# Performance work log

Hardware: AMD Instinct MI355X
Metric: run time of the kernel (lower is better)

## Reference

```python
import jax, jax.numpy as jnp
import numpy as np

B, CIN, COUT, HID, H, W, K, PAD = 16, 64, 64, 32, 32, 32, 5, 2


def self_attention(x, Wq, Wk, Wv):
    # x: [B,C,H,W]; Wq,Wk: [HID,C]; Wv: [C,C]  (1x1 convs as channel matmuls)
    b, c, h, w = x.shape
    n = h * w
    xf = x.reshape(b, c, n)                      # [B,C,N]
    q = jnp.einsum('dc,bcn->bdn', Wq, xf)        # [B,HID,N]
    k = jnp.einsum('dc,bcn->bdn', Wk, xf)        # [B,HID,N]
    v = jnp.einsum('ec,bcn->ben', Wv, xf)        # [B,C,N]
    scores = jnp.einsum('bdn,bdm->bnm', q, k)    # [B,N,N]
    attn = jax.nn.softmax(scores, axis=-1)
    out = jnp.einsum('bcm,bnm->bcn', v, attn)    # aggregate values
    out = out.reshape(b, c, h, w)
    return x + out, attn                          # residual


def conv_lstm_cell(x, h, c, W_lstm, b_lstm):
    combined = jnp.concatenate([x, h], axis=1)   # [B,CIN+COUT,H,W]
    gates = jax.lax.conv_general_dilated(
        combined, W_lstm, window_strides=(1, 1),
        padding=[(PAD, PAD), (PAD, PAD)],
        dimension_numbers=('NCHW', 'OIHW', 'NCHW'))
    gates = gates + b_lstm[None, :, None, None]
    i, f, o, g = jnp.split(gates, 4, axis=1)
    i, f, o = jax.nn.sigmoid(i), jax.nn.sigmoid(f), jax.nn.sigmoid(o)
    g = jnp.tanh(g)
    c_new = f * c + i * g
    h_new = o * jnp.tanh(c_new)
    return h_new, c_new


def setup_inputs() -> dict:
    key = jax.random.key(0)
    ks = jax.random.split(key, 12)
    s = 0.05
    return {
        'x': jax.random.normal(ks[0], (B, CIN, H, W), jnp.float32),
        'h': jax.random.normal(ks[1], (B, COUT, H, W), jnp.float32),
        'c': jax.random.normal(ks[2], (B, COUT, H, W), jnp.float32),
        'Wq_x': jax.random.normal(ks[3], (HID, CIN), jnp.float32) * s,
        'Wk_x': jax.random.normal(ks[4], (HID, CIN), jnp.float32) * s,
        'Wv_x': jax.random.normal(ks[5], (CIN, CIN), jnp.float32) * s,
        'Wq_h': jax.random.normal(ks[6], (HID, COUT), jnp.float32) * s,
        'Wk_h': jax.random.normal(ks[7], (HID, COUT), jnp.float32) * s,
        'Wv_h': jax.random.normal(ks[8], (COUT, COUT), jnp.float32) * s,
        'W_lstm': jax.random.normal(ks[9], (4 * COUT, CIN + COUT, K, K), jnp.float32) * s,
        'b_lstm': jnp.zeros((4 * COUT,), jnp.float32),
    }


def reference(x, h, c, Wq_x, Wk_x, Wv_x, Wq_h, Wk_h, Wv_h, W_lstm, b_lstm):
    X, _ = self_attention(x, Wq_x, Wk_x, Wv_x)
    new_h, new_c = conv_lstm_cell(X, h, c, W_lstm, b_lstm)
    new_h, atten = self_attention(new_h, Wq_h, Wk_h, Wv_h)
    new_h = new_h + new_h  # faithful to `new_h += new_h`
    return new_h, new_c, atten
```

## Files before the change

kernel.cpp:

```cpp
#include <hip/hip_runtime.h>
#include <hip/hip_bf16.h>
#include <cstddef>
#include <cstdint>

#define NTOK 1024
#define NB   16
#define NC   64
#define NHID 32

#define PAD_BSTRIDE 165888
#define PAD_KSTRIDE 82944
#define PAD_BYTES   5308416

typedef __attribute__((ext_vector_type(8))) short short8;
typedef __attribute__((ext_vector_type(4))) float f32x4;

__device__ __forceinline__ ushort f2b(float f) {
  uint32_t u = __builtin_bit_cast(uint32_t, f);
  return (ushort)((u + 0x7FFFu + ((u >> 16) & 1u)) >> 16);
}
__device__ __forceinline__ float b2f(ushort u) {
  return __builtin_bit_cast(float, (uint32_t)u << 16);
}
__device__ __forceinline__ short8 ldw8(const float* __restrict__ p) {
  float4 f0 = *(const float4*)p, f1 = *(const float4*)(p + 4);
  short8 r;
  r[0] = (short)f2b(f0.x); r[1] = (short)f2b(f0.y);
  r[2] = (short)f2b(f0.z); r[3] = (short)f2b(f0.w);
  r[4] = (short)f2b(f1.x); r[5] = (short)f2b(f1.y);
  r[6] = (short)f2b(f1.z); r[7] = (short)f2b(f1.w);
  return r;
}
__device__ __forceinline__ float sigm(float x) { return 1.f / (1.f + __expf(-x)); }
__device__ __forceinline__ float tanh_fast(float x) {
  float e = __expf(2.f * x);
  return 1.f - 2.f / (e + 1.f);
}

__global__ __launch_bounds__(256) void tpose_pad_kernel(
    const float* __restrict__ src, ushort* __restrict__ dst) {
  __shared__ float tile[64][65];
  int t = threadIdx.x;
  int n0 = blockIdx.x * 64, b = blockIdx.y;
  const float* s = src + (size_t)b * NC * NTOK;
#pragma unroll
  for (int r = 0; r < 4; ++r) {
    int c = r * 16 + (t >> 4);
    int nl = (t & 15) * 4;
    float4 v = *(const float4*)(s + (size_t)c * NTOK + n0 + nl);
    tile[c][nl] = v.x; tile[c][nl + 1] = v.y; tile[c][nl + 2] = v.z; tile[c][nl + 3] = v.w;
  }
  __syncthreads();
  int tok = t >> 2, c0 = (t & 3) * 16;
  __attribute__((aligned(16))) ushort tmp[16];
#pragma unroll
  for (int i = 0; i < 16; ++i) tmp[i] = f2b(tile[c0 + i][tok]);
  int gtok = n0 + tok;
  ushort* d = dst + (size_t)b * PAD_BSTRIDE +
              ((gtok >> 5) + 2) * 2304 + ((gtok & 31) + 2) * 64 + c0;
  *(uint4*)(d)     = *(const uint4*)(tmp);
  *(uint4*)(d + 8) = *(const uint4*)(tmp + 8);
}

__global__ __launch_bounds__(256) void qkvproj_kernel(
    const float* __restrict__ x, const float* __restrict__ Wq,
    const float* __restrict__ Wk, const float* __restrict__ Wv,
    ushort* __restrict__ qT, ushort* __restrict__ kT, ushort* __restrict__ vb) {
  __shared__ float tile[64][65];
  __shared__ ushort xb[64][72];
  __shared__ ushort sq[64][32], sk[64][32];
  int t = threadIdx.x, wave = t >> 6, lane = t & 63;
  int lo = lane & 15, lg = lane >> 4;
  int n0 = blockIdx.x * 64, b = blockIdx.y;
  const float* s = x + (size_t)b * NC * NTOK;
#pragma unroll
  for (int r = 0; r < 4; ++r) {
    int c = r * 16 + (t >> 4);
    int nl = (t & 15) * 4;
    float4 v = *(const float4*)(s + (size_t)c * NTOK + n0 + nl);
    tile[c][nl] = v.x; tile[c][nl + 1] = v.y; tile[c][nl + 2] = v.z; tile[c][nl + 3] = v.w;
  }
  __syncthreads();
  {
    int tok = t >> 2, c0 = (t & 3) * 16;
    __attribute__((aligned(16))) ushort tmp[16];
#pragma unroll
    for (int i = 0; i < 16; ++i) tmp[i] = f2b(tile[c0 + i][tok]);
    *(uint4*)(&xb[tok][c0])     = *(const uint4*)(tmp);
    *(uint4*)(&xb[tok][c0 + 8]) = *(const uint4*)(tmp + 8);
  }
  __syncthreads();
  const ushort* xrow = &xb[wave * 16 + lo][8 * lg];
  short8 a0 = *(const short8*)(xrow);
  short8 a1 = *(const short8*)(xrow + 32);
  f32x4 aq[2], ak[2];
#pragma unroll
  for (int dg = 0; dg < 2; ++dg) {
    short8 wq0 = ldw8(Wq + (size_t)(dg * 16 + lo) * NC + 8 * lg);
    short8 wq1 = ldw8(Wq + (size_t)(dg * 16 + lo) * NC + 32 + 8 * lg);
    short8 wk0 = ldw8(Wk + (size_t)(dg * 16 + lo) * NC + 8 * lg);
    short8 wk1 = ldw8(Wk + (size_t)(dg * 16 + lo) * NC + 32 + 8 * lg);
    f32x4 z = {0.f, 0.f, 0.f, 0.f};
    aq[dg] = __builtin_amdgcn_mfma_f32_16x16x32_bf16(a0, wq0, z, 0, 0, 0);
    aq[dg] = __builtin_amdgcn_mfma_f32_16x16x32_bf16(a1, wq1, aq[dg], 0, 0, 0);
    ak[dg] = __builtin_amdgcn_mfma_f32_16x16x32_bf16(a0, wk0, z, 0, 0, 0);
    ak[dg] = __builtin_amdgcn_mfma_f32_16x16x32_bf16(a1, wk1, ak[dg], 0, 0, 0);
  }
  f32x4 av[4];
#pragma unroll
  for (int g = 0; g < 4; ++g) {
    short8 wv0 = ldw8(Wv + (size_t)(g * 16 + lo) * NC + 8 * lg);
    short8 wv1 = ldw8(Wv + (size_t)(g * 16 + lo) * NC + 32 + 8 * lg);
    f32x4 z = {0.f, 0.f, 0.f, 0.f};
    av[g] = __builtin_amdgcn_mfma_f32_16x16x32_bf16(wv0, a0, z, 0, 0, 0);
    av[g] = __builtin_amdgcn_mfma_f32_16x16x32_bf16(wv1, a1, av[g], 0, 0, 0);
  }
#pragma unroll
  for (int dg = 0; dg < 2; ++dg)
#pragma unroll
    for (int r = 0; r < 4; ++r) {
      sq[wave * 16 + 4 * lg + r][dg * 16 + lo] = f2b(aq[dg][r]);
      sk[wave * 16 + 4 * lg + r][dg * 16 + lo] = f2b(ak[dg][r]);
    }
  ushort* vbase = vb + (size_t)b * NC * NTOK + n0 + wave * 16 + lo;
#pragma unroll
  for (int g = 0; g < 4; ++g)
#pragma unroll
    for (int r = 0; r < 4; ++r)
      vbase[(size_t)(g * 16 + lg * 4 + r) * NTOK] = f2b(av[g][r]);
  __syncthreads();
  int tok = t >> 2, d0 = (t & 3) * 8;
  size_t base = ((size_t)b * NTOK + n0 + tok) * NHID + d0;
  *(short8*)(qT + base) = *(const short8*)(&sq[tok][d0]);
  *(short8*)(kT + base) = *(const short8*)(&sk[tok][d0]);
}

#define SP 1048
template <bool ATTN2>
__global__ __launch_bounds__(256) void attn_fused_kernel(
    const ushort* __restrict__ qT, const ushort* __restrict__ kT,
    const ushort* __restrict__ vb, const float* __restrict__ resid,
    float* __restrict__ attnf, float* __restrict__ outf,
    ushort* __restrict__ outb_pad, float scale) {
  __shared__ ushort s_lds[16 * SP];
  __shared__ float wmax[4][16], wsum[4][16];
  int t = threadIdx.x, wave = t >> 6, lane = t & 63;
  int lo = lane & 15, lg = lane >> 4;
  int n0 = blockIdx.x * 16, b = blockIdx.y;
  int m0 = wave * 256;
  short8 a = *(const short8*)(qT + ((size_t)b * NTOK + n0 + lo) * NHID + 8 * lg);
  f32x4 acc[16];
#pragma unroll
  for (int j = 0; j < 16; ++j) {
    short8 bf = *(const short8*)(kT + ((size_t)b * NTOK + m0 + j * 16 + lo) * NHID + 8 * lg);
    f32x4 z = {0.f, 0.f, 0.f, 0.f};
    acc[j] = __builtin_amdgcn_mfma_f32_16x16x32_bf16(a, bf, z, 0, 0, 0);
  }
  float pm[4];
#pragma unroll
  for (int r = 0; r < 4; ++r) {
    float m = acc[0][r];
#pragma unroll
    for (int j = 1; j < 16; ++j) m = fmaxf(m, acc[j][r]);
#pragma unroll
    for (int off = 1; off < 16; off <<= 1) m = fmaxf(m, __shfl_xor(m, off, 64));
    pm[r] = m;
  }
  if (lo == 0)
#pragma unroll
    for (int r = 0; r < 4; ++r) wmax[wave][4 * lg + r] = pm[r];
  __syncthreads();
  float mr[4];
#pragma unroll
  for (int r = 0; r < 4; ++r)
    mr[r] = fmaxf(fmaxf(wmax[0][4 * lg + r], wmax[1][4 * lg + r]),
                  fmaxf(wmax[2][4 * lg + r], wmax[3][4 * lg + r]));
  float ps[4] = {0.f, 0.f, 0.f, 0.f};
#pragma unroll
  for (int j = 0; j < 16; ++j)
#pragma unroll
    for (int r = 0; r < 4; ++r) {
      float e = __expf(acc[j][r] - mr[r]);
      acc[j][r] = e;
      ps[r] += e;
    }
#pragma unroll
  for (int r = 0; r < 4; ++r)
#pragma unroll
    for (int off = 1; off < 16; off <<= 1) ps[r] += __shfl_xor(ps[r], off, 64);
  if (lo == 0)
#pragma unroll
    for (int r = 0; r < 4; ++r) wsum[wave][4 * lg + r] = ps[r];
  __syncthreads();
  float inv[4];
#pragma unroll
  for (int r = 0; r < 4; ++r)
    inv[r] = 1.f / (wsum[0][4 * lg + r] + wsum[1][4 * lg + r] +
                    wsum[2][4 * lg + r] + wsum[3][4 * lg + r]);
#pragma unroll
  for (int j = 0; j < 16; ++j)
#pragma unroll
    for (int r = 0; r < 4; ++r)
      s_lds[(4 * lg + r) * SP + m0 + j * 16 + lo] = f2b(acc[j][r] * inv[r]);
  __syncthreads();
  if constexpr (ATTN2) {
    int ml = lane * 4;
    float* abase = attnf + ((size_t)b * NTOK + n0) * NTOK + m0;
#pragma unroll
    for (int n = 0; n < 16; ++n) {
      ushort4 sv = *(const ushort4*)(s_lds + n * SP + m0 + ml);
      f32x4 o = {b2f(sv.x), b2f(sv.y), b2f(sv.z), b2f(sv.w)};
      __builtin_nontemporal_store(o, (f32x4*)(abase + (size_t)n * NTOK + ml));
    }
  }
  int cb = wave * 16;
  const ushort* vbb = vb + ((size_t)b * NC + cb + lo) * NTOK;
  f32x4 acc2 = {0.f, 0.f, 0.f, 0.f}, acc3 = {0.f, 0.f, 0.f, 0.f};
  for (int ms = 0; ms < NTOK; ms += 64) {
    short8 af0 = *(const short8*)(s_lds + lo * SP + ms + 8 * lg);
    short8 bf0 = *(const short8*)(vbb + ms + 8 * lg);
    short8 af1 = *(const short8*)(s_lds + lo * SP + ms + 32 + 8 * lg);
    short8 bf1 = *(const short8*)(vbb + ms + 32 + 8 * lg);
    acc2 = __builtin_amdgcn_mfma_f32_16x16x32_bf16(af0, bf0, acc2, 0, 0, 0);
    acc3 = __builtin_amdgcn_mfma_f32_16x16x32_bf16(af1, bf1, acc3, 0, 0, 0);
  }
#pragma unroll
  for (int r = 0; r < 4; ++r) acc2[r] += acc3[r];
  int c = cb + lo;
  float4 rv = *(const float4*)(resid + ((size_t)b * NC + c) * NTOK + n0 + 4 * lg);
  float rvv[4] = {rv.x, rv.y, rv.z, rv.w};
  if constexpr (ATTN2) {
    float4 o;
    o.x = scale * (rvv[0] + acc2[0]); o.y = scale * (rvv[1] + acc2[1]);
    o.z = scale * (rvv[2] + acc2[2]); o.w = scale * (rvv[3] + acc2[3]);
    *(float4*)(outf + ((size_t)b * NC + c) * NTOK + n0 + 4 * lg) = o;
  } else {
#pragma unroll
    for (int r = 0; r < 4; ++r) {
      int tok = n0 + 4 * lg + r;
      float val = scale * (rvv[r] + acc2[r]);
      outb_pad[(size_t)b * PAD_BSTRIDE + ((tok >> 5) + 2) * 2304 +
               ((tok & 31) + 2) * 64 + c] = f2b(val);
    }
  }
}

__global__ __launch_bounds__(256) void wpre_kernel(
    const float* __restrict__ W, ushort* __restrict__ Wb) {
  int idx = blockIdx.x * 256 + threadIdx.x;
  const float* src = W + (size_t)idx * 25;
#pragma unroll
  for (int kk = 0; kk < 25; ++kk)
    Wb[((size_t)(idx >> 7) * 25 + kk) * 128 + (idx & 127)] = f2b(src[kk]);
}

#define AP 76
#define BP 76
__global__ __launch_bounds__(256, 2) void conv_lstm_kernel(
    const ushort* __restrict__ pad,
    const ushort* __restrict__ Wb,
    const float* __restrict__ bias, const float* __restrict__ c_in,
    float* __restrict__ c_out, float* __restrict__ h_out) {
  __shared__ ushort ldsA[2][128 * AP];
  __shared__ ushort ldsB[216 * BP];
  int t = threadIdx.x;
  int lane = t & 63, lo = lane & 15, lg = lane >> 4;
  int wid = t >> 6, cb = wid & 1, ph = wid >> 1;
  int pt = blockIdx.x, chh = blockIdx.y, b = blockIdx.z;
  const ushort* pb = pad + (size_t)b * PAD_BSTRIDE + (size_t)(pt * 2) * 2304;

  for (int i = t; i < 1728; i += 256) {
    int pxw = i >> 3, ch8 = (i & 7) * 8;
    uint4 v = *(const uint4*)(pb + (size_t)pxw * 64 + ch8);
    *(uint4*)(ldsB + pxw * BP + ch8) = v;
  }

  const ushort *wsrc0, *wsrc1, *wsrc2, *wsrc3;
  int adst0, adst1, adst2, adst3;
  {
    int i0 = t, i1 = 256 + t, i2 = 512 + t, i3 = 768 + t;
    int r0 = i0 >> 3, r1 = i1 >> 3, r2 = i2 >> 3, r3 = i3 >> 3;
    wsrc0 = Wb + (size_t)((r0 >> 5) * 64 + chh * 32 + (r0 & 31)) * 3200 + (i0 & 7) * 8;
    wsrc1 = Wb + (size_t)((r1 >> 5) * 64 + chh * 32 + (r1 & 31)) * 3200 + (i1 & 7) * 8;
    wsrc2 = Wb + (size_t)((r2 >> 5) * 64 + chh * 32 + (r2 & 31)) * 3200 + (i2 & 7) * 8;
    wsrc3 = Wb + (size_t)((r3 >> 5) * 64 + chh * 32 + (r3 & 31)) * 3200 + (i3 & 7) * 8;
    adst0 = r0 * AP + (i0 & 7) * 8;
    adst1 = r1 * AP + (i1 & 7) * 8;
    adst2 = r2 * AP + (i2 & 7) * 8;
    adst3 = r3 * AP + (i3 & 7) * 8;
  }
  uint4 w0 = *(const uint4*)(wsrc0);
  uint4 w1 = *(const uint4*)(wsrc1);
  uint4 w2 = *(const uint4*)(wsrc2);
  uint4 w3 = *(const uint4*)(wsrc3);

  f32x4 acc[4][2];
#pragma unroll
  for (int i = 0; i < 4; ++i)
#pragma unroll
    for (int j = 0; j < 2; ++j) acc[i][j] = {0.f, 0.f, 0.f, 0.f};

  __syncthreads();
  *(uint4*)(&ldsA[0][adst0]) = w0;
  *(uint4*)(&ldsA[0][adst1]) = w1;
  *(uint4*)(&ldsA[0][adst2]) = w2;
  *(uint4*)(&ldsA[0][adst3]) = w3;
  w0 = *(const uint4*)(wsrc0 + 128);
  w1 = *(const uint4*)(wsrc1 + 128);
  w2 = *(const uint4*)(wsrc2 + 128);
  w3 = *(const uint4*)(wsrc3 + 128);
  __syncthreads();

  for (int s = 0; s < 50; ++s) {
    int cur = s & 1;
    if (s < 49) {
      int nxt = cur ^ 1;
      *(uint4*)(&ldsA[nxt][adst0]) = w0;
      *(uint4*)(&ldsA[nxt][adst1]) = w1;
      *(uint4*)(&ldsA[nxt][adst2]) = w2;
      *(uint4*)(&ldsA[nxt][adst3]) = w3;
      int s2 = (s < 48) ? s + 2 : 49;
      int koff = (s2 < 25) ? s2 * 128 : (s2 - 25) * 128 + 64;
      w0 = *(const uint4*)(wsrc0 + koff);
      w1 = *(const uint4*)(wsrc1 + koff);
      w2 = *(const uint4*)(wsrc2 + koff);
      w3 = *(const uint4*)(wsrc3 + koff);
    }
    int kh = (s >= 25);
    int tap = s - kh * 25;
    int ky = tap / 5, kx = tap - 5 * ky;
    int bbase = (ky * 36 + kx) * BP;
#pragma unroll
    for (int icc = 0; icc < 2; ++icc) {
      short8 af[4], bf[2];
#pragma unroll
      for (int i = 0; i < 4; ++i)
        af[i] = *(const short8*)(&ldsA[cur][(i * 32 + cb * 16 + lo) * AP + icc * 32 + 8 * lg]);
#pragma unroll
      for (int j = 0; j < 2; ++j)
        bf[j] = *(const short8*)(ldsB + bbase + (ph * 36 + j * 16 + lo) * BP + icc * 32 + 8 * lg);
#pragma unroll
      for (int i = 0; i < 4; ++i)
#pragma unroll
        for (int j = 0; j < 2; ++j)
          acc[i][j] = __builtin_amdgcn_mfma_f32_16x16x32_bf16(af[i], bf[j], acc[i][j], 0, 0, 0);
    }
    __syncthreads();
    if (s == 24) {
      for (int i = t; i < 1728; i += 256) {
        int pxw = i >> 3, ch8 = (i & 7) * 8;
        uint4 v = *(const uint4*)(pb + PAD_KSTRIDE + (size_t)pxw * 64 + ch8);
        *(uint4*)(ldsB + pxw * BP + ch8) = v;
      }
      __syncthreads();
    }
  }

#pragma unroll
  for (int j = 0; j < 2; ++j)
#pragma unroll
    for (int r = 0; r < 4; ++r) {
      int ch = chh * 32 + cb * 16 + lg * 4 + r;
      int p = pt * 64 + ph * 32 + j * 16 + lo;
      size_t ci = ((size_t)b * NC + ch) * NTOK + p;
      float iv = sigm(acc[0][j][r] + bias[ch]);
      float fv = sigm(acc[1][j][r] + bias[64 + ch]);
      float ov = sigm(acc[2][j][r] + bias[128 + ch]);
      float gv = tanh_fast(acc[3][j][r] + bias[192 + ch]);
      float cn = fv * c_in[ci] + iv * gv;
      c_out[ci] = cn;
      h_out[ci] = ov * tanh_fast(cn);
    }
}

extern "C" void kernel_launch(void* const* d_in, const int* in_sizes, int n_in,
                              void* d_out, int out_size, void* d_ws, size_t ws_size,
                              hipStream_t stream) {
  const float* x      = (const float*)d_in[0];
  const float* h      = (const float*)d_in[1];
  const float* c      = (const float*)d_in[2];
  const float* Wq_x   = (const float*)d_in[3];
  const float* Wk_x   = (const float*)d_in[4];
  const float* Wv_x   = (const float*)d_in[5];
  const float* Wq_h   = (const float*)d_in[6];
  const float* Wk_h   = (const float*)d_in[7];
  const float* Wv_h   = (const float*)d_in[8];
  const float* W_lstm = (const float*)d_in[9];
  const float* b_lstm = (const float*)d_in[10];

  float* out   = (float*)d_out;
  float* new_h = out;
  float* new_c = out + 1048576;
  float* atten = out + 2097152;

  ushort* wsu = (ushort*)d_ws;
  ushort* qT  = wsu;
  ushort* kT  = wsu + 524288;
  ushort* vb  = wsu + 1048576;

  ushort* Wb    = (ushort*)(atten + 8388608);
  ushort* pad   = (ushort*)(atten + 9437184);
  float*  h_mid = new_h;

  dim3 blk(256);
  (void)hipMemsetAsync(pad, 0, PAD_BYTES, stream);
  qkvproj_kernel<<<dim3(16, NB), blk, 0, stream>>>(x, Wq_x, Wk_x, Wv_x, qT, kT, vb);
  attn_fused_kernel<false><<<dim3(64, NB), blk, 0, stream>>>(
      qT, kT, vb, x, nullptr, nullptr, pad , 1.0f);
  wpre_kernel<<<128, blk, 0, stream>>>(W_lstm, Wb);
  tpose_pad_kernel<<<dim3(16, NB), blk, 0, stream>>>(h, pad + PAD_KSTRIDE);
  conv_lstm_kernel<<<dim3(16, 2, NB), blk, 0, stream>>>(pad, Wb, b_lstm, c, new_c, h_mid);
  qkvproj_kernel<<<dim3(16, NB), blk, 0, stream>>>(h_mid, Wq_h, Wk_h, Wv_h, qT, kT, vb);
  attn_fused_kernel<true><<<dim3(64, NB), blk, 0, stream>>>(
      qT, kT, vb, h_mid, atten, new_h, nullptr, 2.0f);
}
```

Baseline: 127.1 us.

## Stream conv weights via global_load_lds with MFMA-friendly layout; add setprio hints

The weight preprocessing kernel now writes weights in a tap-major, chunk-blocked layout. The conv kernel loads each weight tile straight into LDS with global_load_lds 16-byte copies, replacing the register-staged double buffer, and reads A fragments from the new contiguous layout without padding. s_setprio hints are also wrapped around the MFMA sections in the attention and conv kernels. This frees registers and removes the LDS-store instructions, but correctness now depends on the async LDS loads being waited on before the barrier.

Result: slower. 143.8 us (+13.1%).

```diff
diff --git a/kernel.cpp b/kernel.cpp
--- a/kernel.cpp
+++ b/kernel.cpp
@@ -35,6 +35,11 @@
 __device__ __forceinline__ float tanh_fast(float x) {
   float e = __expf(2.f * x);
   return 1.f - 2.f / (e + 1.f);
+}
+__device__ __forceinline__ void glds16(const ushort* g, ushort* l) {
+  __builtin_amdgcn_global_load_lds(
+      (const __attribute__((address_space(1))) unsigned int*)g,
+      (__attribute__((address_space(3))) unsigned int*)l, 16, 0, 0);
 }
 
 __global__ __launch_bounds__(256) void tpose_pad_kernel(
@@ -150,12 +155,14 @@
   int m0 = wave * 256;
   short8 a = *(const short8*)(qT + ((size_t)b * NTOK + n0 + lo) * NHID + 8 * lg);
   f32x4 acc[16];
+  __builtin_amdgcn_s_setprio(1);
 #pragma unroll
   for (int j = 0; j < 16; ++j) {
     short8 bf = *(const short8*)(kT + ((size_t)b * NTOK + m0 + j * 16 + lo) * NHID + 8 * lg);
     f32x4 z = {0.f, 0.f, 0.f, 0.f};
     acc[j] = __builtin_amdgcn_mfma_f32_16x16x32_bf16(a, bf, z, 0, 0, 0);
   }
+  __builtin_amdgcn_s_setprio(0);
   float pm[4];
 #pragma unroll
   for (int r = 0; r < 4; ++r) {
@@ -216,6 +223,7 @@
   int cb = wave * 16;
   const ushort* vbb = vb + ((size_t)b * NC + cb + lo) * NTOK;
   f32x4 acc2 = {0.f, 0.f, 0.f, 0.f}, acc3 = {0.f, 0.f, 0.f, 0.f};
+  __builtin_amdgcn_s_setprio(1);
   for (int ms = 0; ms < NTOK; ms += 64) {
     short8 af0 = *(const short8*)(s_lds + lo * SP + ms + 8 * lg);
     short8 bf0 = *(const short8*)(vbb + ms + 8 * lg);
@@ -224,6 +232,7 @@
     acc2 = __builtin_amdgcn_mfma_f32_16x16x32_bf16(af0, bf0, acc2, 0, 0, 0);
     acc3 = __builtin_amdgcn_mfma_f32_16x16x32_bf16(af1, bf1, acc3, 0, 0, 0);
   }
+  __builtin_amdgcn_s_setprio(0);
 #pragma unroll
   for (int r = 0; r < 4; ++r) acc2[r] += acc3[r];
   int c = cb + lo;
@@ -248,20 +257,25 @@
 __global__ __launch_bounds__(256) void wpre_kernel(
     const float* __restrict__ W, ushort* __restrict__ Wb) {
   int idx = blockIdx.x * 256 + threadIdx.x;
+  int oc = idx >> 7, ic = idx & 127;
+  int g = oc >> 6, chh = (oc >> 5) & 1, o = oc & 31;
+  int kh = ic >> 6, ic64 = ic & 63;
+  int c = ic64 >> 3;
+  int e = ic64 & 7;
   const float* src = W + (size_t)idx * 25;
-#pragma unroll
-  for (int kk = 0; kk < 25; ++kk)
-    Wb[((size_t)(idx >> 7) * 25 + kk) * 128 + (idx & 127)] = f2b(src[kk]);
-}
-
-#define AP 76
+  for (int kk = 0; kk < 25; ++kk) {
+    size_t dst = ((((size_t)((kk * 2 + kh) * 2 + chh) * 8 + c) * 4 + g) * 32 + o) * 8 + e;
+    Wb[dst] = f2b(src[kk]);
+  }
+}
+
 #define BP 76
 __global__ __launch_bounds__(256, 2) void conv_lstm_kernel(
     const ushort* __restrict__ pad,
     const ushort* __restrict__ Wb,
     const float* __restrict__ bias, const float* __restrict__ c_in,
     float* __restrict__ c_out, float* __restrict__ h_out) {
-  __shared__ ushort ldsA[2][128 * AP];
+  __shared__ ushort ldsA[2][8192];
   __shared__ ushort ldsB[216 * BP];
   int t = threadIdx.x;
   int lane = t & 63, lo = lane & 15, lg = lane >> 4;
@@ -275,24 +289,18 @@
     *(uint4*)(ldsB + pxw * BP + ch8) = v;
   }
 
-  const ushort *wsrc0, *wsrc1, *wsrc2, *wsrc3;
-  int adst0, adst1, adst2, adst3;
-  {
-    int i0 = t, i1 = 256 + t, i2 = 512 + t, i3 = 768 + t;
-    int r0 = i0 >> 3, r1 = i1 >> 3, r2 = i2 >> 3, r3 = i3 >> 3;
-    wsrc0 = Wb + (size_t)((r0 >> 5) * 64 + chh * 32 + (r0 & 31)) * 3200 + (i0 & 7) * 8;
-    wsrc1 = Wb + (size_t)((r1 >> 5) * 64 + chh * 32 + (r1 & 31)) * 3200 + (i1 & 7) * 8;
-    wsrc2 = Wb + (size_t)((r2 >> 5) * 64 + chh * 32 + (r2 & 31)) * 3200 + (i2 & 7) * 8;
-    wsrc3 = Wb + (size_t)((r3 >> 5) * 64 + chh * 32 + (r3 & 31)) * 3200 + (i3 & 7) * 8;
-    adst0 = r0 * AP + (i0 & 7) * 8;
-    adst1 = r1 * AP + (i1 & 7) * 8;
-    adst2 = r2 * AP + (i2 & 7) * 8;
-    adst3 = r3 * AP + (i3 & 7) * 8;
-  }
-  uint4 w0 = *(const uint4*)(wsrc0);
-  uint4 w1 = *(const uint4*)(wsrc1);
-  uint4 w2 = *(const uint4*)(wsrc2);
-  uint4 w3 = *(const uint4*)(wsrc3);
+#define ISSUE_A(buf, sv)                                                       \
+  {                                                                            \
+    int _kh = (sv) >= 25;                                                      \
+    int _tap = (sv) - _kh * 25;                                                \
+    const ushort* _src = Wb + ((size_t)((_tap * 2 + _kh) * 2 + chh)) * 8192 +  \
+                         wid * 2048 + lane * 8;                                \
+    ushort* _dst = &ldsA[buf][wid * 2048];                                     \
+    glds16(_src,        _dst);                                                 \
+    glds16(_src + 512,  _dst + 512);                                           \
+    glds16(_src + 1024, _dst + 1024);                                          \
+    glds16(_src + 1536, _dst + 1536);                                          \
+  }
 
   f32x4 acc[4][2];
 #pragma unroll
@@ -300,42 +308,23 @@
 #pragma unroll
     for (int j = 0; j < 2; ++j) acc[i][j] = {0.f, 0.f, 0.f, 0.f};
 
-  __syncthreads();
-  *(uint4*)(&ldsA[0][adst0]) = w0;
-  *(uint4*)(&ldsA[0][adst1]) = w1;
-  *(uint4*)(&ldsA[0][adst2]) = w2;
-  *(uint4*)(&ldsA[0][adst3]) = w3;
-  w0 = *(const uint4*)(wsrc0 + 128);
-  w1 = *(const uint4*)(wsrc1 + 128);
-  w2 = *(const uint4*)(wsrc2 + 128);
-  w3 = *(const uint4*)(wsrc3 + 128);
+  ISSUE_A(0, 0);
   __syncthreads();
 
   for (int s = 0; s < 50; ++s) {
     int cur = s & 1;
-    if (s < 49) {
-      int nxt = cur ^ 1;
-      *(uint4*)(&ldsA[nxt][adst0]) = w0;
-      *(uint4*)(&ldsA[nxt][adst1]) = w1;
-      *(uint4*)(&ldsA[nxt][adst2]) = w2;
-      *(uint4*)(&ldsA[nxt][adst3]) = w3;
-      int s2 = (s < 48) ? s + 2 : 49;
-      int koff = (s2 < 25) ? s2 * 128 : (s2 - 25) * 128 + 64;
-      w0 = *(const uint4*)(wsrc0 + koff);
-      w1 = *(const uint4*)(wsrc1 + koff);
-      w2 = *(const uint4*)(wsrc2 + koff);
-      w3 = *(const uint4*)(wsrc3 + koff);
-    }
+    if (s < 49) ISSUE_A(cur ^ 1, s + 1);
     int kh = (s >= 25);
     int tap = s - kh * 25;
     int ky = tap / 5, kx = tap - 5 * ky;
     int bbase = (ky * 36 + kx) * BP;
+    __builtin_amdgcn_s_setprio(1);
 #pragma unroll
     for (int icc = 0; icc < 2; ++icc) {
       short8 af[4], bf[2];
 #pragma unroll
       for (int i = 0; i < 4; ++i)
-        af[i] = *(const short8*)(&ldsA[cur][(i * 32 + cb * 16 + lo) * AP + icc * 32 + 8 * lg]);
+        af[i] = *(const short8*)(&ldsA[cur][((icc * 4 + lg) * 4 + i) * 256 + (cb * 16 + lo) * 8]);
 #pragma unroll
       for (int j = 0; j < 2; ++j)
         bf[j] = *(const short8*)(ldsB + bbase + (ph * 36 + j * 16 + lo) * BP + icc * 32 + 8 * lg);
@@ -345,6 +334,7 @@
         for (int j = 0; j < 2; ++j)
           acc[i][j] = __builtin_amdgcn_mfma_f32_16x16x32_bf16(af[i], bf[j], acc[i][j], 0, 0, 0);
     }
+    __builtin_amdgcn_s_setprio(0);
     __syncthreads();
     if (s == 24) {
       for (int i = t; i < 1728; i += 256) {
@@ -355,6 +345,7 @@
       __syncthreads();
     }
   }
+#undef ISSUE_A
 
 #pragma unroll
   for (int j = 0; j < 2; ++j)
```
